# Performance work log

Measured on AMD Instinct MI355X. Metric: run time of the kernel, lower is better.

## Reference

```python
import jax, jax.numpy as jnp
import numpy as np

D = 1024    # n_embd
H = 16      # n_heads
HD = D // H # head_dim
E = 8       # n_experts
K = 2       # k_best
DFF = 4096  # expert hidden
EPS = 1e-6
TEMP = 1.0  # target_temperature


def rmsnorm(x, w):
    return x * jax.lax.rsqrt(jnp.mean(x * x, axis=-1, keepdims=True) + EPS) * w


def setup_inputs() -> dict:
    key = jax.random.key(0)
    ks = jax.random.split(key, 10)
    B, S = 2, 2048
    s = 0.02
    return {
        "x": jax.random.normal(ks[0], (B, S, D), jnp.float32),
        "attention_mask": jnp.ones((B, S), jnp.int32),
        "attn_norm_w": jnp.ones((D,), jnp.float32),
        "wq": jax.random.normal(ks[1], (D, D), jnp.float32) * s,
        "wk": jax.random.normal(ks[2], (D, D), jnp.float32) * s,
        "wv": jax.random.normal(ks[3], (D, D), jnp.float32) * s,
        "wo": jax.random.normal(ks[4], (D, D), jnp.float32) * s,
        "mlp_norm_w": jnp.ones((D,), jnp.float32),
        "router_w": jax.random.normal(ks[5], (D, E), jnp.float32) * s,
        "w1": jax.random.normal(ks[6], (E, D, DFF), jnp.float32) * s,
        "b1": jnp.zeros((E, DFF), jnp.float32),
        "w2": jax.random.normal(ks[7], (E, DFF, D), jnp.float32) * s,
        "b2": jnp.zeros((E, D), jnp.float32),
    }


def reference(x, attention_mask, attn_norm_w, wq, wk, wv, wo, mlp_norm_w,
              router_w, w1, b1, w2, b2):
    B, S, _ = x.shape
    # ---- attention sub-block ----
    residual = x
    h = rmsnorm(x, attn_norm_w)
    q = (h @ wq).reshape(B, S, H, HD).transpose(0, 2, 1, 3)  # bhsd
    k = (h @ wk).reshape(B, S, H, HD).transpose(0, 2, 1, 3)
    v = (h @ wv).reshape(B, S, H, HD).transpose(0, 2, 1, 3)
    scores = jnp.einsum('bhqd,bhkd->bhqk', q, k) / np.sqrt(HD).astype(np.float32)
    causal = jnp.tril(jnp.ones((S, S), bool))
    mask = causal[None, None, :, :] & (attention_mask[:, None, None, :] > 0)
    scores = jnp.where(mask, scores, jnp.float32(-1e9))
    attn = jax.nn.softmax(scores, axis=-1)
    o = jnp.einsum('bhqk,bhkd->bhqd', attn, v).transpose(0, 2, 1, 3).reshape(B, S, D) @ wo
    x = residual + o

    # ---- MoE sub-block ----
    residual = x
    h = rmsnorm(x, mlp_norm_w)
    logits = h @ router_w                        # (B,S,E)
    probs = jax.nn.softmax(logits / TEMP, axis=-1)
    top_k_scores, top_k_indices = jax.lax.top_k(probs, K)  # (B,S,K)
    sel = jax.nn.one_hot(top_k_indices, E, dtype=probs.dtype)  # (B,S,K,E)
    expert_counts = sel.sum(axis=(0, 1, 2))      # (E,)
    frac = expert_counts / (B * S * K)
    balancing_loss = E * jnp.sum(frac * probs.mean(axis=(0, 1)))

    T = B * S
    flat = h.reshape(T, D)
    # dense per-expert MLP over all tokens, then gather the routed slots
    hid = jax.nn.gelu(jnp.einsum('td,edf->etf', flat, w1) + b1[:, None, :])  # (E,T,DFF)
    all_y = jnp.einsum('etf,efd->etd', hid, w2) + b2[:, None, :]             # (E,T,D)
    idx = top_k_indices.reshape(T, K)
    expert_out = all_y[idx, jnp.arange(T)[:, None], :]  # (T,K,D)
    # faithful to torch: outputs.view(k, B, S, D) is a raw reinterpretation
    out = expert_out.reshape(K, B, S, D)
    w = top_k_scores.transpose(2, 0, 1)[..., None]  # (K,B,S,1)
    x = residual + (out * w).sum(axis=0)
    return (x, balancing_loss, expert_counts)
```

## Files before the change

kernel.cpp:

```cpp
#include <hip/hip_runtime.h>


typedef _Float16 f16;
typedef _Float16 f16x8 __attribute__((ext_vector_type(8)));
typedef _Float16 f16x4v __attribute__((ext_vector_type(4)));
typedef float f32x4 __attribute__((ext_vector_type(4)));

#define DMODEL 1024
#define NHEAD  16
#define HDIM   64
#define NEXP   8
#define DFFN   4096
#define NBATCH 2
#define NSEQ   2048
#define NTOK   4096
#define NPAIR  8192

#define OFF_WQKVT  0ull
#define OFF_WOT    6291456ull
#define OFF_W1T    8388608ull
#define OFF_W2T    75497472ull
#define OFF_HATTN  142606336ull
#define OFF_Q      150994944ull
#define OFF_K      159383552ull
#define OFF_VT     167772160ull
#define OFF_OC     176160768ull
#define OFF_XMID   184549376ull
#define OFF_HMLP   201326592ull
#define OFF_HID    209715200ull
#define OFF_Y      276824064ull
#define OFF_LIST   310378496ull
#define OFF_METAE  310509568ull
#define OFF_METAP  310542336ull
#define OFF_METAS  310575104ull
#define OFF_BPSUM  310607872ull
#define OFF_CNT    310640640ull
#define OFF_PSUM   310640704ull
#define OFF_BASE   310640768ull

__device__ __forceinline__ void ldsAsync16(const void* g, void* l) {
  __builtin_amdgcn_global_load_lds((const __attribute__((address_space(1))) void*)g,
                                   (__attribute__((address_space(3))) void*)l, 16, 0, 0);
}

__global__ void transpose_cast_kernel(const float* __restrict__ src, f16* __restrict__ dst,
                                      int R, int C) {
  __shared__ float tile[32][33];
  const size_t zoff = (size_t)blockIdx.z * R * C;
  src += zoff; dst += zoff;
  int c0 = blockIdx.x * 32, r0 = blockIdx.y * 32;
  int tx = threadIdx.x, ty = threadIdx.y;
#pragma unroll
  for (int i = 0; i < 4; i++)
    tile[ty + i * 8][tx] = src[(size_t)(r0 + ty + i * 8) * C + c0 + tx];
  __syncthreads();
#pragma unroll
  for (int i = 0; i < 4; i++)
    dst[(size_t)(c0 + ty + i * 8) * R + r0 + tx] = (f16)tile[tx][ty + i * 8];
}

__global__ void rmsnorm_kernel(const float* __restrict__ x, const float* __restrict__ w,
                               f16* __restrict__ out) {
  int t = blockIdx.x, tid = threadIdx.x;
  float4 v = ((const float4*)(x + (size_t)t * DMODEL))[tid];
  float ss = v.x * v.x + v.y * v.y + v.z * v.z + v.w * v.w;
#pragma unroll
  for (int o = 32; o > 0; o >>= 1) ss += __shfl_down(ss, o);
  __shared__ float red[4];
  if ((tid & 63) == 0) red[tid >> 6] = ss;
  __syncthreads();
  float tot = red[0] + red[1] + red[2] + red[3];
  float rstd = rsqrtf(tot / (float)DMODEL + 1e-6f);
  float4 wv = ((const float4*)w)[tid];
  f16x4v o4;
  o4[0] = (f16)(v.x * rstd * wv.x);
  o4[1] = (f16)(v.y * rstd * wv.y);
  o4[2] = (f16)(v.z * rstd * wv.z);
  o4[3] = (f16)(v.w * rstd * wv.w);
  *(f16x4v*)(out + (size_t)t * DMODEL + tid * 4) = o4;
}

template <class EPI>
__device__ __forceinline__ void gemm128(const f16* aP0, const f16* aP1, const f16* aP2, const f16* aP3,
                                        const f16* bP0, const f16* bP1, const f16* bP2, const f16* bP3,
                                        int K, EPI epi) {
  __shared__ __align__(16) f16 sA[128 * 64];
  __shared__ __align__(16) f16 sB[128 * 64];
  const int tid = threadIdx.x;
  const int lane = tid & 63, wave = tid >> 6;
  const int wm = (wave >> 1) * 64, wn = (wave & 1) * 64;
  const int q4 = lane >> 4, l15 = lane & 15;
  const f16* aP[4] = {aP0, aP1, aP2, aP3};
  const f16* bP[4] = {bP0, bP1, bP2, bP3};
  f32x4 zero = {0.f, 0.f, 0.f, 0.f};
  f32x4 acc[4][4];
#pragma unroll
  for (int i = 0; i < 4; i++)
#pragma unroll
    for (int j = 0; j < 4; j++) acc[i][j] = zero;

  for (int k0 = 0; k0 < K; k0 += 64) {
    __syncthreads();
#pragma unroll
    for (int i = 0; i < 4; i++) {
      ldsAsync16(aP[i] + k0, &sA[(i * 4 + wave) * 512]);
      ldsAsync16(bP[i] + k0, &sB[(i * 4 + wave) * 512]);
    }
    __syncthreads();
#pragma unroll
    for (int kk = 0; kk < 2; kk++) {
      f16x8 af[4], bf[4];
#pragma unroll
      for (int mi = 0; mi < 4; mi++)
        af[mi] = *(const f16x8*)&sA[(wm + mi * 16 + l15) * 64 + kk * 32 + q4 * 8];
#pragma unroll
      for (int ni = 0; ni < 4; ni++)
        bf[ni] = *(const f16x8*)&sB[(wn + ni * 16 + l15) * 64 + kk * 32 + q4 * 8];
#pragma unroll
      for (int mi = 0; mi < 4; mi++)
#pragma unroll
        for (int ni = 0; ni < 4; ni++)
          acc[mi][ni] = __builtin_amdgcn_mfma_f32_16x16x32_f16(af[mi], bf[ni], acc[mi][ni], 0, 0, 0);
    }
  }
#pragma unroll
  for (int mi = 0; mi < 4; mi++)
#pragma unroll
    for (int ni = 0; ni < 4; ni++)
#pragma unroll
      for (int r = 0; r < 4; r++)
        epi(wm + mi * 16 + q4 * 4 + r, wn + ni * 16 + l15, acc[mi][ni][r]);
}

__global__ __launch_bounds__(256, 2) void gemm_qkv_kernel(
    const f16* __restrict__ hA, const f16* __restrict__ wT,
    f16* __restrict__ qb, f16* __restrict__ kb, f16* __restrict__ vtb) {
  int mt = blockIdx.y, nt = blockIdx.x;
  int tid = threadIdx.x, lane = tid & 63, wave = tid >> 6;
  int kc = lane & 7, rs = lane >> 3;
  const f16 *a[4], *b[4];
#pragma unroll
  for (int i = 0; i < 4; i++) {
    int row = i * 32 + wave * 8 + rs;
    a[i] = hA + (size_t)(mt * 128 + row) * DMODEL + kc * 8;
    b[i] = wT + (size_t)(nt * 128 + row) * DMODEL + kc * 8;
  }
  int mB = mt * 128, nB = nt * 128;
  gemm128(a[0], a[1], a[2], a[3], b[0], b[1], b[2], b[3], DMODEL,
    [&](int r, int c, float v) {
      int m = mB + r, n = nB + c;
      int mat = n >> 10, nn = n & 1023;
      int h = nn >> 6, d = nn & 63;
      int bI = m >> 11, s = m & 2047;
      int bh = bI * NHEAD + h;
      f16 hv = (f16)v;
      if (mat == 0)      qb[((size_t)bh * NSEQ + s) * HDIM + d] = hv;
      else if (mat == 1) kb[((size_t)bh * NSEQ + s) * HDIM + d] = hv;
      else               vtb[((size_t)bh * HDIM + d) * NSEQ + s] = hv;
    });
}

__global__ __launch_bounds__(256, 2) void gemm_o_kernel(
    const f16* __restrict__ oc, const f16* __restrict__ woT,
    const float* __restrict__ xin, float* __restrict__ xmid) {
  int mt = blockIdx.y, nt = blockIdx.x;
  int tid = threadIdx.x, lane = tid & 63, wave = tid >> 6;
  int kc = lane & 7, rs = lane >> 3;
  const f16 *a[4], *b[4];
#pragma unroll
  for (int i = 0; i < 4; i++) {
    int row = i * 32 + wave * 8 + rs;
    a[i] = oc + (size_t)(mt * 128 + row) * DMODEL + kc * 8;
    b[i] = woT + (size_t)(nt * 128 + row) * DMODEL + kc * 8;
  }
  int mB = mt * 128, nB = nt * 128;
  gemm128(a[0], a[1], a[2], a[3], b[0], b[1], b[2], b[3], DMODEL,
    [&](int r, int c, float v) {
      size_t idx = (size_t)(mB + r) * DMODEL + nB + c;
      xmid[idx] = xin[idx] + v;
    });
}

__global__ __launch_bounds__(256, 2) void gemm_moe1_kernel(
    const f16* __restrict__ hM, const f16* __restrict__ w1T, const float* __restrict__ b1,
    const int* __restrict__ cnt, const int* __restrict__ base, const int* __restrict__ list,
    f16* __restrict__ hid) {
  int e = blockIdx.z, mt = blockIdx.y, nt = blockIdx.x;
  int c_e = cnt[e];
  if (mt * 128 >= c_e) return;
  int tid = threadIdx.x, lane = tid & 63, wave = tid >> 6;
  int kc = lane & 7, rs = lane >> 3;
  const f16 *a[4], *b[4];
#pragma unroll
  for (int i = 0; i < 4; i++) {
    int row = i * 32 + wave * 8 + rs;
    int rr = mt * 128 + row; rr = rr < c_e ? rr : c_e - 1;
    int tok = list[e * NTOK + rr];
    a[i] = hM + (size_t)tok * DMODEL + kc * 8;
    b[i] = w1T + ((size_t)e * DFFN + nt * 128 + row) * DMODEL + kc * 8;
  }
  int rowBase = base[e] + mt * 128, nB = nt * 128, mLoc = mt * 128;
  gemm128(a[0], a[1], a[2], a[3], b[0], b[1], b[2], b[3], DMODEL,
    [&](int r, int c, float v) {
      if (mLoc + r < c_e) {
        float v2 = v + b1[e * DFFN + nB + c];
        float u = 1.5957691216057308f * (v2 + 0.044715f * v2 * v2 * v2);
        float th = 1.f - 2.f / (__expf(u) + 1.f);
        hid[(size_t)(rowBase + r) * DFFN + nB + c] = (f16)(0.5f * v2 * (1.f + th));
      }
    });
}

__global__ __launch_bounds__(256, 2) void gemm_moe2_kernel(
    const f16* __restrict__ hid, const f16* __restrict__ w2T, const float* __restrict__ b2,
    const int* __restrict__ cnt, const int* __restrict__ base, float* __restrict__ y) {
  int e = blockIdx.z, mt = blockIdx.y, nt = blockIdx.x;
  int c_e = cnt[e];
  if (mt * 128 >= c_e) return;
  int tid = threadIdx.x, lane = tid & 63, wave = tid >> 6;
  int kc = lane & 7, rs = lane >> 3;
  int bse = base[e];
  const f16 *a[4], *b[4];
#pragma unroll
  for (int i = 0; i < 4; i++) {
    int row = i * 32 + wave * 8 + rs;
    int rr = mt * 128 + row; rr = rr < c_e ? rr : c_e - 1;
    a[i] = hid + (size_t)(bse + rr) * DFFN + kc * 8;
    b[i] = w2T + ((size_t)e * DMODEL + nt * 128 + row) * DFFN + kc * 8;
  }
  int nB = nt * 128, mLoc = mt * 128;
  gemm128(a[0], a[1], a[2], a[3], b[0], b[1], b[2], b[3], DFFN,
    [&](int r, int c, float v) {
      if (mLoc + r < c_e)
        y[(size_t)(bse + mLoc + r) * DMODEL + nB + c] = v + b2[e * DMODEL + nB + c];
    });
}

__global__ __launch_bounds__(256, 4) void attn_kernel(
    const f16* __restrict__ qb, const f16* __restrict__ kb, const f16* __restrict__ vtb,
    const int* __restrict__ amask, f16* __restrict__ oc) {
  int bh = blockIdx.x, qt = blockIdx.y;
  int bI = bh >> 4, h = bh & 15;
  int qbase = qt * 64;
  int tid = threadIdx.x, lane = tid & 63, wave = tid >> 6;
  int q4 = lane >> 4, l15 = lane & 15;
  int kc = lane & 7, rs = lane >> 3;

  __shared__ __align__(16) f16 sQ[64 * 64];
  __shared__ __align__(16) f16 sK[64 * 64];
  __shared__ __align__(16) f16 sVT[64 * 64];
  __shared__ __align__(16) f16 sP[4][16 * 64];
  __shared__ int sMask[64];

  const f16* qBH = qb + (size_t)bh * NSEQ * HDIM;
  const f16* kBH = kb + (size_t)bh * NSEQ * HDIM;
  const f16* vBH = vtb + (size_t)bh * HDIM * NSEQ;

#pragma unroll
  for (int i = 0; i < 2; i++) {
    int row = i * 32 + wave * 8 + rs;
    ldsAsync16(qBH + (size_t)(qbase + row) * HDIM + kc * 8, &sQ[(i * 4 + wave) * 512]);
  }

  f32x4 zero = {0.f, 0.f, 0.f, 0.f};
  f32x4 accO[4];
  float mrow[4], lrow[4];
#pragma unroll
  for (int j = 0; j < 4; j++) { accO[j] = zero; mrow[j] = -3.0e38f; lrow[j] = 0.f; }

  f16* sPw = sP[wave];

  for (int kt = 0; kt <= qt; kt++) {
    int kb0 = kt * 64;
    bool diag = (kt == qt);
    __syncthreads();
#pragma unroll
    for (int i = 0; i < 2; i++) {
      int row = i * 32 + wave * 8 + rs;
      ldsAsync16(kBH + (size_t)(kb0 + row) * HDIM + kc * 8, &sK[(i * 4 + wave) * 512]);
      ldsAsync16(vBH + (size_t)row * NSEQ + kb0 + kc * 8, &sVT[(i * 4 + wave) * 512]);
    }
    if (tid < 64) sMask[tid] = amask[bI * NSEQ + kb0 + tid];
    __syncthreads();

    f32x4 accS[4];
#pragma unroll
    for (int j = 0; j < 4; j++) accS[j] = zero;
#pragma unroll
    for (int kk = 0; kk < 2; kk++) {
      f16x8 af = *(const f16x8*)&sQ[(wave * 16 + l15) * 64 + kk * 32 + q4 * 8];
      f16x8 bf[4];
#pragma unroll
      for (int nj = 0; nj < 4; nj++)
        bf[nj] = *(const f16x8*)&sK[(nj * 16 + l15) * 64 + kk * 32 + q4 * 8];
#pragma unroll
      for (int nj = 0; nj < 4; nj++)
        accS[nj] = __builtin_amdgcn_mfma_f32_16x16x32_f16(af, bf[nj], accS[nj], 0, 0, 0);
    }
    bool mok[4];
    int gk[4];
#pragma unroll
    for (int nj = 0; nj < 4; nj++) {
      gk[nj] = nj * 16 + l15;
      mok[nj] = sMask[gk[nj]] > 0;
    }
#pragma unroll
    for (int r = 0; r < 4; r++) {
      int lq = wave * 16 + q4 * 4 + r;
      float rm = -3.0e38f;
#pragma unroll
      for (int nj = 0; nj < 4; nj++) {
        float s = accS[nj][r] * 0.125f;
        bool ok = mok[nj] && (!diag || gk[nj] <= lq);
        s = ok ? s : -1.0e9f;
        accS[nj][r] = s;
        rm = fmaxf(rm, s);
      }
#pragma unroll
      for (int o = 1; o < 16; o <<= 1) rm = fmaxf(rm, __shfl_xor(rm, o));
      float mold = mrow[r];
      float mnew = fmaxf(mold, rm);
      float alpha = __expf(mold - mnew);
      float rsum = 0.f;
#pragma unroll
      for (int nj = 0; nj < 4; nj++) {
        float p = __expf(accS[nj][r] - mnew);
        rsum += p;
        sPw[(q4 * 4 + r) * 64 + nj * 16 + l15] = (f16)p;
      }
#pragma unroll
      for (int o = 1; o < 16; o <<= 1) rsum += __shfl_xor(rsum, o);
      lrow[r] = lrow[r] * alpha + rsum;
      mrow[r] = mnew;
#pragma unroll
      for (int dj = 0; dj < 4; dj++) accO[dj][r] *= alpha;
    }
#pragma unroll
    for (int kk = 0; kk < 2; kk++) {
      f16x8 pf = *(const f16x8*)&sPw[l15 * 64 + kk * 32 + q4 * 8];
      f16x8 vf[4];
#pragma unroll
      for (int dj = 0; dj < 4; dj++)
        vf[dj] = *(const f16x8*)&sVT[(dj * 16 + l15) * 64 + kk * 32 + q4 * 8];
#pragma unroll
      for (int dj = 0; dj < 4; dj++)
        accO[dj] = __builtin_amdgcn_mfma_f32_16x16x32_f16(pf, vf[dj], accO[dj], 0, 0, 0);
    }
  }
#pragma unroll
  for (int r = 0; r < 4; r++) {
    float inv = 1.f / lrow[r];
    int s = qbase + wave * 16 + q4 * 4 + r;
    size_t rowoff = ((size_t)bI * NSEQ + s) * DMODEL + h * HDIM;
#pragma unroll
    for (int dj = 0; dj < 4; dj++)
      oc[rowoff + dj * 16 + l15] = (f16)(accO[dj][r] * inv);
  }
}

__global__ __launch_bounds__(256) void router_kernel(
    const float* __restrict__ xmid, const float* __restrict__ normw,
    const float* __restrict__ rw, int2* __restrict__ metaE,
    float2* __restrict__ metaS, float* __restrict__ blockpsum) {
  int wave = threadIdx.x >> 6, lane = threadIdx.x & 63;
  int t = blockIdx.x * 4 + wave;
  __shared__ float sprob[4][8];

  const float4* xr = (const float4*)(xmid + (size_t)t * DMODEL);
  const float4* wr = (const float4*)normw;
  float4 v[4];
  float ss = 0.f;
#pragma unroll
  for (int i = 0; i < 4; i++) {
    v[i] = xr[lane * 4 + i];
    ss += v[i].x * v[i].x + v[i].y * v[i].y + v[i].z * v[i].z + v[i].w * v[i].w;
  }
#pragma unroll
  for (int o = 32; o > 0; o >>= 1) ss += __shfl_xor(ss, o);
  float rstd = rsqrtf(ss / (float)DMODEL + 1e-6f);

  float part[8] = {0, 0, 0, 0, 0, 0, 0, 0};
#pragma unroll
  for (int i = 0; i < 4; i++) {
    float4 wv = wr[lane * 4 + i];
    float hv[4] = {v[i].x * rstd * wv.x, v[i].y * rstd * wv.y,
                   v[i].z * rstd * wv.z, v[i].w * rstd * wv.w};
#pragma unroll
    for (int j = 0; j < 4; j++) {
      int row = lane * 16 + i * 4 + j;
      const float4* rr = (const float4*)(rw + (size_t)row * NEXP);
      float4 a = rr[0], b = rr[1];
      part[0] += hv[j] * a.x; part[1] += hv[j] * a.y;
      part[2] += hv[j] * a.z; part[3] += hv[j] * a.w;
      part[4] += hv[j] * b.x; part[5] += hv[j] * b.y;
      part[6] += hv[j] * b.z; part[7] += hv[j] * b.w;
    }
  }
#pragma unroll
  for (int o = 1; o < 64; o <<= 1)
#pragma unroll
    for (int e = 0; e < 8; e++) part[e] += __shfl_xor(part[e], o);

  if (lane == 0) {
    float mx = -3.0e38f;
#pragma unroll
    for (int e = 0; e < 8; e++) mx = fmaxf(mx, part[e]);
    float probs[8], sum = 0.f;
#pragma unroll
    for (int e = 0; e < 8; e++) { probs[e] = __expf(part[e] - mx); sum += probs[e]; }
    float inv = 1.f / sum;
#pragma unroll
    for (int e = 0; e < 8; e++) { probs[e] *= inv; sprob[wave][e] = probs[e]; }
    int e0 = 0;
#pragma unroll
    for (int e = 1; e < 8; e++) if (part[e] > part[e0]) e0 = e;
    int e1 = (e0 == 0) ? 1 : 0;
#pragma unroll
    for (int e = 0; e < 8; e++) if (e != e0 && part[e] > part[e1]) e1 = e;
    metaE[t] = make_int2(e0, e1);
    metaS[t] = make_float2(probs[e0], probs[e1]);
  }
  __syncthreads();
  if (threadIdx.x < 8)
    blockpsum[blockIdx.x * 8 + threadIdx.x] =
        sprob[0][threadIdx.x] + sprob[1][threadIdx.x] +
        sprob[2][threadIdx.x] + sprob[3][threadIdx.x];
}

__global__ __launch_bounds__(256) void scatter_kernel(
    const int2* __restrict__ metaE, int* __restrict__ list,
    int* __restrict__ metaP, int* __restrict__ cnt) {
  int e = blockIdx.x;
  int tid = threadIdx.x, lane = tid & 63, w = tid >> 6;
  __shared__ int wsum[4];
  __shared__ int sbase;
  if (tid == 0) sbase = 0;
  __syncthreads();
  for (int c = 0; c < NTOK; c += 256) {
    int tok = c + tid;
    int2 me = metaE[tok];
    bool m0 = (me.x == e), m1 = (me.y == e);
    bool m = m0 || m1;
    unsigned long long mask = __ballot(m);
    int wpre = __popcll(mask & ((1ull << lane) - 1ull));
    if (lane == 0) wsum[w] = __popcll(mask);
    __syncthreads();
    int base0 = sbase;
    int pre = wpre;
    for (int i = 0; i < w; i++) pre += wsum[i];
    int tot = wsum[0] + wsum[1] + wsum[2] + wsum[3];
    if (m) {
      int pos = base0 + pre;
      list[e * NTOK + base0 + pre] = tok;
      metaP[tok * 2 + (m0 ? 0 : 1)] = pos;
    }
    __syncthreads();
    if (tid == 0) sbase = base0 + tot;
  }
  __syncthreads();
  if (tid == 0) cnt[e] = sbase;
}

__global__ __launch_bounds__(256) void finalize_kernel(
    const int* __restrict__ cnt, const float* __restrict__ blockpsum,
    int* __restrict__ base, float* __restrict__ out_tail) {
  int tid = threadIdx.x;
  int e = tid & 7, slot = tid >> 3;
  float acc = 0.f;
  for (int i = slot; i < 1024; i += 32) acc += blockpsum[i * 8 + e];
  __shared__ float red[256];
  red[tid] = acc;
  __syncthreads();
  for (int s = 128; s >= 8; s >>= 1) {
    if (tid < s) red[tid] += red[tid + s];
    __syncthreads();
  }
  if (tid == 0) {
    int b = 0;
#pragma unroll
    for (int i = 0; i < 8; i++) { base[i] = b; b += cnt[i]; }
    base[8] = b;
    float loss = 0.f;
#pragma unroll
    for (int i = 0; i < 8; i++)
      loss += ((float)cnt[i] / (float)NPAIR) * (red[i] / (float)NTOK);
    out_tail[0] = loss * (float)NEXP;
#pragma unroll
    for (int i = 0; i < 8; i++) out_tail[1 + i] = (float)cnt[i];
  }
}

__global__ void combine_kernel(const float* __restrict__ xmid, const float* __restrict__ yv,
                               const int2* __restrict__ metaE, const int* __restrict__ metaP,
                               const float2* __restrict__ metaS,
                               const int* __restrict__ base, float* __restrict__ out) {
  int t = blockIdx.x, tid = threadIdx.x;
  int2 me = metaE[t];
  float2 sc = metaS[t];
  size_t s0 = (size_t)(base[me.x] + metaP[t * 2 + 0]) * DMODEL;
  size_t s1 = (size_t)(base[me.y] + metaP[t * 2 + 1]) * DMODEL;
  float4 a = ((const float4*)(xmid + (size_t)t * DMODEL))[tid];
  float4 y0 = ((const float4*)(yv + s0))[tid];
  float4 y1 = ((const float4*)(yv + s1))[tid];
  float4 o;
  o.x = a.x + sc.x * y0.x + sc.y * y1.x;
  o.y = a.y + sc.x * y0.y + sc.y * y1.y;
  o.z = a.z + sc.x * y0.z + sc.y * y1.z;
  o.w = a.w + sc.x * y0.w + sc.y * y1.w;
  ((float4*)(out + (size_t)t * DMODEL))[tid] = o;
}

extern "C" void kernel_launch(void* const* d_in, const int* in_sizes, int n_in,
                              void* d_out, int out_size, void* d_ws, size_t ws_size,
                              hipStream_t stream) {
  (void)in_sizes; (void)n_in; (void)out_size; (void)ws_size;
  const float* x    = (const float*)d_in[0];
  const int*   am   = (const int*)d_in[1];
  const float* anw  = (const float*)d_in[2];
  const float* wq   = (const float*)d_in[3];
  const float* wk   = (const float*)d_in[4];
  const float* wv   = (const float*)d_in[5];
  const float* wo   = (const float*)d_in[6];
  const float* mnw  = (const float*)d_in[7];
  const float* rw   = (const float*)d_in[8];
  const float* w1   = (const float*)d_in[9];
  const float* b1   = (const float*)d_in[10];
  const float* w2   = (const float*)d_in[11];
  const float* b2   = (const float*)d_in[12];
  float* out = (float*)d_out;
  char* ws = (char*)d_ws;

  f16* wqkvT = (f16*)(ws + OFF_WQKVT);
  f16* woT   = (f16*)(ws + OFF_WOT);
  f16* w1T   = (f16*)(ws + OFF_W1T);
  f16* w2T   = (f16*)(ws + OFF_W2T);
  f16* hattn = (f16*)(ws + OFF_HATTN);
  f16* qb    = (f16*)(ws + OFF_Q);
  f16* kb    = (f16*)(ws + OFF_K);
  f16* vtb   = (f16*)(ws + OFF_VT);
  f16* oc    = (f16*)(ws + OFF_OC);
  float* xmid = (float*)(ws + OFF_XMID);
  f16* hmlp  = (f16*)(ws + OFF_HMLP);
  f16* hid   = (f16*)(ws + OFF_HID);
  float* y   = (float*)(ws + OFF_Y);
  int* list  = (int*)(ws + OFF_LIST);
  int2* metaE = (int2*)(ws + OFF_METAE);
  int* metaP  = (int*)(ws + OFF_METAP);
  float2* metaS = (float2*)(ws + OFF_METAS);
  float* bpsum = (float*)(ws + OFF_BPSUM);
  int* cnt   = (int*)(ws + OFF_CNT);
  int* base  = (int*)(ws + OFF_BASE);

  dim3 tb(32, 8, 1);
  transpose_cast_kernel<<<dim3(32, 32, 1), tb, 0, stream>>>(wq, wqkvT, 1024, 1024);
  transpose_cast_kernel<<<dim3(32, 32, 1), tb, 0, stream>>>(wk, wqkvT + 1024 * 1024, 1024, 1024);
  transpose_cast_kernel<<<dim3(32, 32, 1), tb, 0, stream>>>(wv, wqkvT + 2 * 1024 * 1024, 1024, 1024);
  transpose_cast_kernel<<<dim3(32, 32, 1), tb, 0, stream>>>(wo, woT, 1024, 1024);
  transpose_cast_kernel<<<dim3(128, 32, 8), tb, 0, stream>>>(w1, w1T, 1024, 4096);
  transpose_cast_kernel<<<dim3(32, 128, 8), tb, 0, stream>>>(w2, w2T, 4096, 1024);

  rmsnorm_kernel<<<NTOK, 256, 0, stream>>>(x, anw, hattn);
  gemm_qkv_kernel<<<dim3(24, 32), 256, 0, stream>>>(hattn, wqkvT, qb, kb, vtb);
  attn_kernel<<<dim3(32, 32), 256, 0, stream>>>(qb, kb, vtb, am, oc);
  gemm_o_kernel<<<dim3(8, 32), 256, 0, stream>>>(oc, woT, x, xmid);
  rmsnorm_kernel<<<NTOK, 256, 0, stream>>>(xmid, mnw, hmlp);
  router_kernel<<<1024, 256, 0, stream>>>(xmid, mnw, rw, metaE, metaS, bpsum);
  scatter_kernel<<<8, 256, 0, stream>>>(metaE, list, metaP, cnt);
  finalize_kernel<<<1, 256, 0, stream>>>(cnt, bpsum, base, out + (size_t)NTOK * DMODEL);
  gemm_moe1_kernel<<<dim3(32, 32, 8), 256, 0, stream>>>(hmlp, w1T, b1, cnt, base, list, hid);
  gemm_moe2_kernel<<<dim3(8, 32, 8), 256, 0, stream>>>(hid, w2T, b2, cnt, base, y);
  combine_kernel<<<NTOK, 256, 0, stream>>>(xmid, y, metaE, metaP, metaS, base, out);
}
```

Before: 863.5 us.

## Swizzle LDS tiles to avoid bank conflicts and split-K the MoE down-projection

Applies an XOR swizzle to the 16-byte chunk positions in the shared-memory A/B tiles of the common GEMM routine. This is meant to reduce LDS bank conflicts when MFMA fragments are read. The second MoE GEMM is split into two K halves that write separate partial outputs, which doubles the number of active blocks for better CU occupancy. The combine kernel sums the two partials, adding extra memory traffic and a 32MB buffer that aliases dead attention workspace.

```diff
diff --git a/kernel.cpp b/kernel.cpp
--- a/kernel.cpp
+++ b/kernel.cpp
@@ -29,6 +29,7 @@
 #define OFF_HMLP   201326592ull
 #define OFF_HID    209715200ull
 #define OFF_Y      276824064ull
+#define OFF_Y2     OFF_HATTN
 #define OFF_LIST   310378496ull
 #define OFF_METAE  310509568ull
 #define OFF_METAP  310542336ull
@@ -90,6 +91,7 @@
   const int lane = tid & 63, wave = tid >> 6;
   const int wm = (wave >> 1) * 64, wn = (wave & 1) * 64;
   const int q4 = lane >> 4, l15 = lane & 15;
+  const int sw = lane & 7;
   const f16* aP[4] = {aP0, aP1, aP2, aP3};
   const f16* bP[4] = {bP0, bP1, bP2, bP3};
   f32x4 zero = {0.f, 0.f, 0.f, 0.f};
@@ -110,12 +112,13 @@
 #pragma unroll
     for (int kk = 0; kk < 2; kk++) {
       f16x8 af[4], bf[4];
+      int jx = ((kk * 4 + q4) ^ sw) * 8;
 #pragma unroll
       for (int mi = 0; mi < 4; mi++)
-        af[mi] = *(const f16x8*)&sA[(wm + mi * 16 + l15) * 64 + kk * 32 + q4 * 8];
+        af[mi] = *(const f16x8*)&sA[(wm + mi * 16 + l15) * 64 + jx];
 #pragma unroll
       for (int ni = 0; ni < 4; ni++)
-        bf[ni] = *(const f16x8*)&sB[(wn + ni * 16 + l15) * 64 + kk * 32 + q4 * 8];
+        bf[ni] = *(const f16x8*)&sB[(wn + ni * 16 + l15) * 64 + jx];
 #pragma unroll
       for (int mi = 0; mi < 4; mi++)
 #pragma unroll
@@ -138,12 +141,13 @@
   int mt = blockIdx.y, nt = blockIdx.x;
   int tid = threadIdx.x, lane = tid & 63, wave = tid >> 6;
   int kc = lane & 7, rs = lane >> 3;
+  int kcs = (kc ^ rs) * 8;
   const f16 *a[4], *b[4];
 #pragma unroll
   for (int i = 0; i < 4; i++) {
     int row = i * 32 + wave * 8 + rs;
-    a[i] = hA + (size_t)(mt * 128 + row) * DMODEL + kc * 8;
-    b[i] = wT + (size_t)(nt * 128 + row) * DMODEL + kc * 8;
+    a[i] = hA + (size_t)(mt * 128 + row) * DMODEL + kcs;
+    b[i] = wT + (size_t)(nt * 128 + row) * DMODEL + kcs;
   }
   int mB = mt * 128, nB = nt * 128;
   gemm128(a[0], a[1], a[2], a[3], b[0], b[1], b[2], b[3], DMODEL,
@@ -166,12 +170,13 @@
   int mt = blockIdx.y, nt = blockIdx.x;
   int tid = threadIdx.x, lane = tid & 63, wave = tid >> 6;
   int kc = lane & 7, rs = lane >> 3;
+  int kcs = (kc ^ rs) * 8;
   const f16 *a[4], *b[4];
 #pragma unroll
   for (int i = 0; i < 4; i++) {
     int row = i * 32 + wave * 8 + rs;
-    a[i] = oc + (size_t)(mt * 128 + row) * DMODEL + kc * 8;
-    b[i] = woT + (size_t)(nt * 128 + row) * DMODEL + kc * 8;
+    a[i] = oc + (size_t)(mt * 128 + row) * DMODEL + kcs;
+    b[i] = woT + (size_t)(nt * 128 + row) * DMODEL + kcs;
   }
   int mB = mt * 128, nB = nt * 128;
   gemm128(a[0], a[1], a[2], a[3], b[0], b[1], b[2], b[3], DMODEL,
@@ -190,14 +195,15 @@
   if (mt * 128 >= c_e) return;
   int tid = threadIdx.x, lane = tid & 63, wave = tid >> 6;
   int kc = lane & 7, rs = lane >> 3;
+  int kcs = (kc ^ rs) * 8;
   const f16 *a[4], *b[4];
 #pragma unroll
   for (int i = 0; i < 4; i++) {
     int row = i * 32 + wave * 8 + rs;
     int rr = mt * 128 + row; rr = rr < c_e ? rr : c_e - 1;
     int tok = list[e * NTOK + rr];
-    a[i] = hM + (size_t)tok * DMODEL + kc * 8;
-    b[i] = w1T + ((size_t)e * DFFN + nt * 128 + row) * DMODEL + kc * 8;
+    a[i] = hM + (size_t)tok * DMODEL + kcs;
+    b[i] = w1T + ((size_t)e * DFFN + nt * 128 + row) * DMODEL + kcs;
   }
   int rowBase = base[e] + mt * 128, nB = nt * 128, mLoc = mt * 128;
   gemm128(a[0], a[1], a[2], a[3], b[0], b[1], b[2], b[3], DMODEL,
@@ -213,26 +219,32 @@
 
 __global__ __launch_bounds__(256, 2) void gemm_moe2_kernel(
     const f16* __restrict__ hid, const f16* __restrict__ w2T, const float* __restrict__ b2,
-    const int* __restrict__ cnt, const int* __restrict__ base, float* __restrict__ y) {
-  int e = blockIdx.z, mt = blockIdx.y, nt = blockIdx.x;
+    const int* __restrict__ cnt, const int* __restrict__ base,
+    float* __restrict__ y, float* __restrict__ y2) {
+  int z = blockIdx.z, e = z >> 1, kh = z & 1;
+  int mt = blockIdx.y, nt = blockIdx.x;
   int c_e = cnt[e];
   if (mt * 128 >= c_e) return;
   int tid = threadIdx.x, lane = tid & 63, wave = tid >> 6;
   int kc = lane & 7, rs = lane >> 3;
+  int kcs = (kc ^ rs) * 8 + kh * 2048;
   int bse = base[e];
   const f16 *a[4], *b[4];
 #pragma unroll
   for (int i = 0; i < 4; i++) {
     int row = i * 32 + wave * 8 + rs;
     int rr = mt * 128 + row; rr = rr < c_e ? rr : c_e - 1;
-    a[i] = hid + (size_t)(bse + rr) * DFFN + kc * 8;
-    b[i] = w2T + ((size_t)e * DMODEL + nt * 128 + row) * DFFN + kc * 8;
+    a[i] = hid + (size_t)(bse + rr) * DFFN + kcs;
+    b[i] = w2T + ((size_t)e * DMODEL + nt * 128 + row) * DFFN + kcs;
   }
   int nB = nt * 128, mLoc = mt * 128;
-  gemm128(a[0], a[1], a[2], a[3], b[0], b[1], b[2], b[3], DFFN,
+  float* yo = kh ? y2 : y;
+  gemm128(a[0], a[1], a[2], a[3], b[0], b[1], b[2], b[3], 2048,
     [&](int r, int c, float v) {
-      if (mLoc + r < c_e)
-        y[(size_t)(bse + mLoc + r) * DMODEL + nB + c] = v + b2[e * DMODEL + nB + c];
+      if (mLoc + r < c_e) {
+        float bias = kh ? 0.f : b2[e * DMODEL + nB + c];
+        yo[(size_t)(bse + mLoc + r) * DMODEL + nB + c] = v + bias;
+      }
     });
 }
 
@@ -491,6 +503,7 @@
 }
 
 __global__ void combine_kernel(const float* __restrict__ xmid, const float* __restrict__ yv,
+                               const float* __restrict__ yv2,
                                const int2* __restrict__ metaE, const int* __restrict__ metaP,
                                const float2* __restrict__ metaS,
                                const int* __restrict__ base, float* __restrict__ out) {
@@ -500,13 +513,15 @@
   size_t s0 = (size_t)(base[me.x] + metaP[t * 2 + 0]) * DMODEL;
   size_t s1 = (size_t)(base[me.y] + metaP[t * 2 + 1]) * DMODEL;
   float4 a = ((const float4*)(xmid + (size_t)t * DMODEL))[tid];
-  float4 y0 = ((const float4*)(yv + s0))[tid];
-  float4 y1 = ((const float4*)(yv + s1))[tid];
+  float4 y0a = ((const float4*)(yv + s0))[tid];
+  float4 y0b = ((const float4*)(yv2 + s0))[tid];
+  float4 y1a = ((const float4*)(yv + s1))[tid];
+  float4 y1b = ((const float4*)(yv2 + s1))[tid];
   float4 o;
-  o.x = a.x + sc.x * y0.x + sc.y * y1.x;
-  o.y = a.y + sc.x * y0.y + sc.y * y1.y;
-  o.z = a.z + sc.x * y0.z + sc.y * y1.z;
-  o.w = a.w + sc.x * y0.w + sc.y * y1.w;
+  o.x = a.x + sc.x * (y0a.x + y0b.x) + sc.y * (y1a.x + y1b.x);
+  o.y = a.y + sc.x * (y0a.y + y0b.y) + sc.y * (y1a.y + y1b.y);
+  o.z = a.z + sc.x * (y0a.z + y0b.z) + sc.y * (y1a.z + y1b.z);
+  o.w = a.w + sc.x * (y0a.w + y0b.w) + sc.y * (y1a.w + y1b.w);
   ((float4*)(out + (size_t)t * DMODEL))[tid] = o;
 }
 
@@ -543,6 +558,7 @@
   f16* hmlp  = (f16*)(ws + OFF_HMLP);
   f16* hid   = (f16*)(ws + OFF_HID);
   float* y   = (float*)(ws + OFF_Y);
+  float* y2  = (float*)(ws + OFF_Y2);
   int* list  = (int*)(ws + OFF_LIST);
   int2* metaE = (int2*)(ws + OFF_METAE);
   int* metaP  = (int*)(ws + OFF_METAP);
@@ -568,6 +584,6 @@
   scatter_kernel<<<8, 256, 0, stream>>>(metaE, list, metaP, cnt);
   finalize_kernel<<<1, 256, 0, stream>>>(cnt, bpsum, base, out + (size_t)NTOK * DMODEL);
   gemm_moe1_kernel<<<dim3(32, 32, 8), 256, 0, stream>>>(hmlp, w1T, b1, cnt, base, list, hid);
-  gemm_moe2_kernel<<<dim3(8, 32, 8), 256, 0, stream>>>(hid, w2T, b2, cnt, base, y);
-  combine_kernel<<<NTOK, 256, 0, stream>>>(xmid, y, metaE, metaP, metaS, base, out);
-}
+  gemm_moe2_kernel<<<dim3(8, 32, 16), 256, 0, stream>>>(hid, w2T, b2, cnt, base, y, y2);
+  combine_kernel<<<NTOK, 256, 0, stream>>>(xmid, y, y2, metaE, metaP, metaS, base, out);
+}
```

Result: faster. 835.8 us (-3.2%).
